# Optimization experiments

Measured on AMD Instinct MI355X. Metric: run time of the kernel, lower is better.

The kernel has to match this reference:

```python
import jax, jax.numpy as jnp
import numpy as np

G = 32               # sdf grid resolution (grid_size init default)
SCALE_FACTOR = 0.2   # forward default scale_factor
EPS = 1e-12


def setup_inputs() -> dict:
    key = jax.random.key(0)
    k1, k2 = jax.random.split(key)
    H, V, F = 2, 778, 1538  # two hands, MANO topology
    vertices = jax.random.normal(k1, (H, V, 3), dtype=jnp.float32)
    faces = jax.random.randint(k2, (F, 3), 0, V, dtype=jnp.int32)
    return {"vertices": vertices, "faces": faces}


def _sdiv(n, d):
    return n / jnp.where(jnp.abs(d) < EPS, EPS, d)


def _point_tri_dist2(p, a, b, c):
    # p: [P,1,3]; a,b,c: [1,F,3] -> squared distance [P,F] (Ericson closest-point)
    ab = b - a; ac = c - a; ap = p - a
    d1 = jnp.sum(ab * ap, -1); d2 = jnp.sum(ac * ap, -1)
    bp = p - b; d3 = jnp.sum(ab * bp, -1); d4 = jnp.sum(ac * bp, -1)
    cp = p - c; d5 = jnp.sum(ab * cp, -1); d6 = jnp.sum(ac * cp, -1)
    vc = d1 * d4 - d3 * d2
    vb = d5 * d2 - d1 * d6
    va = d3 * d6 - d5 * d4
    denom = va + vb + vc
    v_in = _sdiv(vb, denom); w_in = _sdiv(vc, denom)
    res = a + ab * v_in[..., None] + ac * w_in[..., None]  # face interior
    # edge BC
    cond = ((va <= 0) & ((d4 - d3) >= 0) & ((d5 - d6) >= 0))[..., None]
    w = _sdiv(d4 - d3, (d4 - d3) + (d5 - d6))[..., None]
    res = jnp.where(cond, b + (c - b) * w, res)
    # edge AC
    cond = ((vb <= 0) & (d2 >= 0) & (d6 <= 0))[..., None]
    w = _sdiv(d2, d2 - d6)[..., None]
    res = jnp.where(cond, a + ac * w, res)
    # edge AB
    cond = ((vc <= 0) & (d1 >= 0) & (d3 <= 0))[..., None]
    w = _sdiv(d1, d1 - d3)[..., None]
    res = jnp.where(cond, a + ab * w, res)
    # vertex regions (highest precedence)
    res = jnp.where(((d6 >= 0) & (d5 <= d6))[..., None], jnp.broadcast_to(c, res.shape), res)
    res = jnp.where(((d3 >= 0) & (d4 <= d3))[..., None], jnp.broadcast_to(b, res.shape), res)
    res = jnp.where(((d1 <= 0) & (d2 <= 0))[..., None], jnp.broadcast_to(a, res.shape), res)
    return jnp.sum((p - res) ** 2, -1)


def _inside(p, a, b, c):
    # parity of +x ray intersections (Moller-Trumbore with dir = (1,0,0))
    e1 = b - a; e2 = c - a
    det = e1[..., 1] * (-e2[..., 2]) + e1[..., 2] * e2[..., 1]  # dot(e1, cross(dir,e2))
    inv = _sdiv(1.0, det)
    s = p - a
    u = (s[..., 1] * (-e2[..., 2]) + s[..., 2] * e2[..., 1]) * inv
    q = jnp.cross(s, e1)
    v = q[..., 0] * inv                # dot(dir, q)
    t = jnp.sum(e2 * q, -1) * inv
    hit = (jnp.abs(det) > 1e-9) & (u >= 0) & (u <= 1) & (v >= 0) & (u + v <= 1) & (t > 0)
    return (jnp.sum(hit.astype(jnp.int32), axis=-1) % 2) == 1


def _sdf_grid(tri):
    # tri: [F,3,3] scaled triangles -> phi [G,G,G] laid out [z,y,x] (grid_sample DHW)
    a = tri[None, :, 0]; b = tri[None, :, 1]; c = tri[None, :, 2]
    lin = jnp.linspace(-1.0, 1.0, G, dtype=tri.dtype)
    zz, yy, xx = jnp.meshgrid(lin, lin, lin, indexing='ij')
    pts = jnp.stack([xx, yy, zz], -1).reshape(G, G * G, 3)  # chunk over z-slabs

    def slab(ps):
        p = ps[:, None, :]
        d2 = jnp.min(_point_tri_dist2(p, a, b, c), axis=1)
        ins = _inside(p, a, b, c)
        return jnp.where(ins, jnp.sqrt(jnp.maximum(d2, 0.0)), 0.0)

    return jax.lax.map(slab, pts).reshape(G, G, G)


def _trilinear(phi, coords):
    # grid_sample(align_corners=True, padding_mode='zeros'), coords [N,3] in xyz order
    g = G - 1
    f = (coords + 1.0) * 0.5 * g
    fx, fy, fz = f[:, 0], f[:, 1], f[:, 2]
    x0f = jnp.floor(fx); y0f = jnp.floor(fy); z0f = jnp.floor(fz)
    wx = fx - x0f; wy = fy - y0f; wz = fz - z0f
    x0 = x0f.astype(jnp.int32); y0 = y0f.astype(jnp.int32); z0 = z0f.astype(jnp.int32)

    def corner(zi, yi, xi, w):
        valid = (zi >= 0) & (zi <= g) & (yi >= 0) & (yi <= g) & (xi >= 0) & (xi <= g)
        val = phi[jnp.clip(zi, 0, g), jnp.clip(yi, 0, g), jnp.clip(xi, 0, g)]
        return jnp.where(valid, val, 0.0) * w

    out = (corner(z0, y0, x0, (1 - wz) * (1 - wy) * (1 - wx))
           + corner(z0, y0, x0 + 1, (1 - wz) * (1 - wy) * wx)
           + corner(z0, y0 + 1, x0, (1 - wz) * wy * (1 - wx))
           + corner(z0, y0 + 1, x0 + 1, (1 - wz) * wy * wx)
           + corner(z0 + 1, y0, x0, wz * (1 - wy) * (1 - wx))
           + corner(z0 + 1, y0, x0 + 1, wz * (1 - wy) * wx)
           + corner(z0 + 1, y0 + 1, x0, wz * wy * (1 - wx))
           + corner(z0 + 1, y0 + 1, x0 + 1, wz * wy * wx))
    return out


def reference(vertices, faces):
    H = vertices.shape[0]
    bmin = vertices.min(axis=1)   # [H,3]
    bmax = vertices.max(axis=1)
    center = jax.lax.stop_gradient(((bmin + bmax) * 0.5)[:, None, :])           # [H,1,3]
    scale = jax.lax.stop_gradient(
        ((1.0 + SCALE_FACTOR) * 0.5 * (bmax - bmin).max(-1))[:, None, None])    # [H,1,1]
    v_scaled = jax.lax.stop_gradient((vertices - center) / scale)
    tris = v_scaled[:, faces]                                                    # [H,F,3,3]
    phi = jax.lax.stop_gradient(jax.vmap(_sdf_grid)(tris))                       # [H,G,G,G]
    i = 1  # hardcoded loop 'for i in [1]' in the source
    coords = ((vertices - center[i][None]) / scale[i][None]).reshape(-1, 3)
    phi_val = _trilinear(phi[i], coords).reshape(H, -1)
    weights = jnp.ones((H, 1), dtype=vertices.dtype).at[i, 0].set(0.0)
    loss = jnp.sum(weights * phi_val) / (H ** 2)
    return loss
```

## Files before the change

### kernel.cpp

```cpp
#include <hip/hip_runtime.h>
#include <math.h>

#define NNODE 32768
#define NTHR  256
#define CHUNK 128
#define GY    160

__device__ __forceinline__ float rguard(float d) {
    float dd = (fabsf(d) < 1e-12f) ? 1e-12f : d;
    return __builtin_amdgcn_rcpf(dd);
}

__device__ __forceinline__ void cell_of(float px, float py, float pz,
                                        int& x0, int& y0, int& z0,
                                        float& wx, float& wy, float& wz) {
#pragma clang fp contract(off)
    float fx = (px + 1.0f) * 0.5f * 31.0f;
    float fy = (py + 1.0f) * 0.5f * 31.0f;
    float fz = (pz + 1.0f) * 0.5f * 31.0f;
    float x0f = floorf(fx), y0f = floorf(fy), z0f = floorf(fz);
    wx = fx - x0f; wy = fy - y0f; wz = fz - z0f;
    x0 = (int)fmaxf(fminf(x0f, 33.0f), -2.0f);
    y0 = (int)fmaxf(fminf(y0f, 33.0f), -2.0f);
    z0 = (int)fmaxf(fminf(z0f, 33.0f), -2.0f);
}

__device__ __forceinline__ void bbox_of(const float* __restrict__ verts, int V,
                                        float& ocx, float& ocy, float& ocz,
                                        float& osc) {
#pragma clang fp contract(off)
    const float* v1 = verts + (size_t)V * 3;
    float mn[3] = {1e30f, 1e30f, 1e30f};
    float mx[3] = {-1e30f, -1e30f, -1e30f};
    for (int i = threadIdx.x; i < V; i += blockDim.x) {
        for (int c = 0; c < 3; ++c) {
            float val = v1[i * 3 + c];
            mn[c] = fminf(mn[c], val);
            mx[c] = fmaxf(mx[c], val);
        }
    }
    for (int off = 32; off >= 1; off >>= 1) {
        for (int c = 0; c < 3; ++c) {
            mn[c] = fminf(mn[c], __shfl_down(mn[c], off));
            mx[c] = fmaxf(mx[c], __shfl_down(mx[c], off));
        }
    }
    __shared__ float smn[16][3], smx[16][3];
    int wv = threadIdx.x >> 6, lane = threadIdx.x & 63;
    if (lane == 0)
        for (int c = 0; c < 3; ++c) { smn[wv][c] = mn[c]; smx[wv][c] = mx[c]; }
    __syncthreads();
    const int nw = (int)blockDim.x >> 6;
    float ext = -1e30f, cc[3];
    for (int c = 0; c < 3; ++c) {
        float lo = 1e30f, hi = -1e30f;
        for (int w = 0; w < nw; ++w) {
            lo = fminf(lo, smn[w][c]);
            hi = fmaxf(hi, smx[w][c]);
        }
        cc[c] = (lo + hi) * 0.5f;
        ext = fmaxf(ext, hi - lo);
    }
    ocx = cc[0]; ocy = cc[1]; ocz = cc[2];
    osc = (1.0f + 0.2f) * 0.5f * ext;
    __syncthreads();
}

__device__ __forceinline__ void tri_node(
        float ax, float ay, float az, float abx, float aby, float abz,
        float acx, float acy, float acz, float inv, float det,
        float dbb, float dbc, float dcc,
        float px, float py, float pz, float& mind2, int& h) {
    float apx = px - ax, apy = py - ay, apz = pz - az;
    {
#pragma clang fp contract(fast)
        float d1 = abx * apx + aby * apy + abz * apz;
        float d2 = acx * apx + acy * apy + acz * apz;
        float d3 = d1 - dbb;
        float d4 = d2 - dbc;
        float d5 = d1 - dbc;
        float d6 = d2 - dcc;
        float vc = d1 * d4 - d3 * d2;
        float vb = d5 * d2 - d1 * d6;
        float va = d3 * d6 - d5 * d4;
        float denom = va + vb + vc;
        float rd = rguard(denom);
        float v_in = vb * rd, w_in = vc * rd;
        float rx = ax + abx * v_in + acx * w_in;
        float ry = ay + aby * v_in + acy * w_in;
        float rz = az + abz * v_in + acz * w_in;
        if (va <= 0.0f && (d4 - d3) >= 0.0f && (d5 - d6) >= 0.0f) {
            float w2 = (d4 - d3) * rguard((d4 - d3) + (d5 - d6));
            rx = ax + abx + (acx - abx) * w2;
            ry = ay + aby + (acy - aby) * w2;
            rz = az + abz + (acz - abz) * w2;
        }
        if (vb <= 0.0f && d2 >= 0.0f && d6 <= 0.0f) {
            float w2 = d2 * rguard(d2 - d6);
            rx = ax + acx * w2; ry = ay + acy * w2; rz = az + acz * w2;
        }
        if (vc <= 0.0f && d1 >= 0.0f && d3 <= 0.0f) {
            float w2 = d1 * rguard(d1 - d3);
            rx = ax + abx * w2; ry = ay + aby * w2; rz = az + abz * w2;
        }
        if (d6 >= 0.0f && d5 <= d6) { rx = ax + acx; ry = ay + acy; rz = az + acz; }
        if (d3 >= 0.0f && d4 <= d3) { rx = ax + abx; ry = ay + aby; rz = az + abz; }
        if (d1 <= 0.0f && d2 <= 0.0f) { rx = ax; ry = ay; rz = az; }
        float ddx = px - rx, ddy = py - ry, ddz = pz - rz;
        mind2 = fminf(mind2, ddx * ddx + ddy * ddy + ddz * ddz);
    }
    {
#pragma clang fp contract(off)
        float u = (apy * (-acz) + apz * acy) * inv;
        float qx = apy * abz - apz * aby;
        float qy = apz * abx - apx * abz;
        float qz = apx * aby - apy * abx;
        float v = qx * inv;
        float tt = (acx * qx + acy * qy + acz * qz) * inv;
        h += (fabsf(det) > 1e-9f && u >= 0.0f && u <= 1.0f && v >= 0.0f &&
              (u + v) <= 1.0f && tt > 0.0f) ? 1 : 0;
    }
}

__global__ void __launch_bounds__(NTHR) k_setup(
        const float* __restrict__ verts, const int* __restrict__ faces,
        float* __restrict__ tri, unsigned int* __restrict__ d2b,
        int* __restrict__ hits, int* __restrict__ cnt, int* __restrict__ list,
        int V, int F) {
    float cx0, cy0, cz0, sc;
    bbox_of(verts, V, cx0, cy0, cz0, sc);
    const int b = (int)blockIdx.x, tid = threadIdx.x;

    for (int t = b * NTHR + tid; t < NNODE; t += (int)gridDim.x * NTHR) {
        d2b[t] = 0xFFFFFFFFu;
        hits[t] = 0;
    }

    if (b == 0) {
        __shared__ unsigned bm[NNODE / 32];
        __shared__ int scnt[NTHR];
        for (int k = 0; k < 4; ++k) bm[tid * 4 + k] = 0u;
        __syncthreads();
        for (int i = tid; i < V; i += NTHR) {
#pragma clang fp contract(off)
            float px = (verts[i * 3 + 0] - cx0) / sc;
            float py = (verts[i * 3 + 1] - cy0) / sc;
            float pz = (verts[i * 3 + 2] - cz0) / sc;
            int x0, y0, z0; float wx, wy, wz;
            cell_of(px, py, pz, x0, y0, z0, wx, wy, wz);
            for (int k = 0; k < 8; ++k) {
                int zi = z0 + ((k >> 2) & 1), yi = y0 + ((k >> 1) & 1),
                    xi = x0 + (k & 1);
                if ((unsigned)zi < 32u && (unsigned)yi < 32u && (unsigned)xi < 32u) {
                    int node = (zi * 32 + yi) * 32 + xi;
                    atomicOr(&bm[node >> 5], 1u << (node & 31));
                }
            }
        }
        __syncthreads();
        unsigned w0 = bm[tid * 4 + 0], w1 = bm[tid * 4 + 1],
                 w2 = bm[tid * 4 + 2], w3 = bm[tid * 4 + 3];
        int c = __popc(w0) + __popc(w1) + __popc(w2) + __popc(w3);
        scnt[tid] = c;
        __syncthreads();
        for (int off = 1; off < NTHR; off <<= 1) {
            int v_ = (tid >= off) ? scnt[tid - off] : 0;
            __syncthreads();
            scnt[tid] += v_;
            __syncthreads();
        }
        if (tid == NTHR - 1) cnt[0] = scnt[NTHR - 1];
        int off = scnt[tid] - c;
        unsigned wsv[4] = {w0, w1, w2, w3};
        for (int k = 0; k < 4; ++k) {
            unsigned w = wsv[k];
            int basebit = (tid * 4 + k) * 32;
            while (w) {
                int bb = __ffs(w) - 1;
                list[off++] = basebit + bb;
                w &= w - 1;
            }
        }
    } else {
        int f = (b - 1) * NTHR + tid;
        if (f < F) {
#pragma clang fp contract(off)
            const float* v1 = verts + (size_t)V * 3;
            int i0 = faces[f * 3 + 0], i1 = faces[f * 3 + 1], i2 = faces[f * 3 + 2];
            float ax = (v1[i0 * 3 + 0] - cx0) / sc, ay = (v1[i0 * 3 + 1] - cy0) / sc,
                  az = (v1[i0 * 3 + 2] - cz0) / sc;
            float bx = (v1[i1 * 3 + 0] - cx0) / sc, by = (v1[i1 * 3 + 1] - cy0) / sc,
                  bz = (v1[i1 * 3 + 2] - cz0) / sc;
            float cx = (v1[i2 * 3 + 0] - cx0) / sc, cy = (v1[i2 * 3 + 1] - cy0) / sc,
                  cz = (v1[i2 * 3 + 2] - cz0) / sc;
            float abx = bx - ax, aby = by - ay, abz = bz - az;
            float acx = cx - ax, acy = cy - ay, acz = cz - az;
            float det = aby * (-acz) + abz * acy;
            float dd = (fabsf(det) < 1e-12f) ? 1e-12f : det;
            float inv = 1.0f / dd;
            float* r = tri + (size_t)f * 16;
            r[0] = ax;  r[1] = ay;  r[2] = az;
            r[3] = abx; r[4] = aby; r[5] = abz;
            r[6] = acx; r[7] = acy; r[8] = acz;
            r[9] = inv; r[10] = det;
            r[11] = abx * abx + aby * aby + abz * abz;
            r[12] = abx * acx + aby * acy + abz * acz;
            r[13] = acx * acx + acy * acy + acz * acz;
            r[14] = 0.0f; r[15] = 0.0f;
        }
    }
}

__global__ void __launch_bounds__(NTHR) k_main(
        const float* __restrict__ tri, const int* __restrict__ list,
        const int* __restrict__ cnt, unsigned int* __restrict__ d2b,
        int* __restrict__ hits, int F) {
    __shared__ float s[14][CHUNK];
    const int tid = threadIdx.x, lane = tid & 63, wv = tid >> 6;
    const int cbase = (int)blockIdx.x * CHUNK;
    const int tn = min(CHUNK, F - cbase);

    if (tid < tn) {
        const float4* g = (const float4*)(tri + (size_t)(cbase + tid) * 16);
        float4 r0 = g[0], r1 = g[1], r2 = g[2], r3 = g[3];
        s[0][tid] = r0.x;  s[1][tid] = r0.y;  s[2][tid] = r0.z;  s[3][tid] = r0.w;
        s[4][tid] = r1.x;  s[5][tid] = r1.y;  s[6][tid] = r1.z;  s[7][tid] = r1.w;
        s[8][tid] = r2.x;  s[9][tid] = r2.y;  s[10][tid] = r2.z; s[11][tid] = r2.w;
        s[12][tid] = r3.x; s[13][tid] = r3.y;
    }
    __syncthreads();

    const int n = cnt[0];
    const int ngroups = (n + 3) >> 2;
    for (int g = (int)blockIdx.y; g < ngroups; g += (int)gridDim.y) {
        const int idx = g * 4 + wv;
        if (idx >= n) continue;
        const int node = list[idx];
        float px, py, pz;
        {
#pragma clang fp contract(off)
            px = (float)((double)(node & 31) * (2.0 / 31.0) - 1.0);
            py = (float)((double)((node >> 5) & 31) * (2.0 / 31.0) - 1.0);
            pz = (float)((double)(node >> 10) * (2.0 / 31.0) - 1.0);
        }
        float m = 1e30f;
        int h = 0;
        for (int mi = 0; mi * 64 < tn; ++mi) {
            int j = lane + mi * 64;
            if (j < tn) {
                tri_node(s[0][j], s[1][j], s[2][j], s[3][j], s[4][j], s[5][j],
                         s[6][j], s[7][j], s[8][j], s[9][j], s[10][j],
                         s[11][j], s[12][j], s[13][j], px, py, pz, m, h);
            }
        }
        for (int off = 32; off >= 1; off >>= 1) {
            m = fminf(m, __shfl_xor(m, off));
            h += __shfl_xor(h, off);
        }
        if (lane == 0) {
            atomicMin(d2b + node, __float_as_uint(m));
            atomicAdd(hits + node, h);
        }
    }
}

__global__ void k_sum(const float* __restrict__ verts,
                      const unsigned int* __restrict__ d2b, const int* __restrict__ hits,
                      float* __restrict__ out, int V) {
    float cx, cy, cz, sc;
    bbox_of(verts, V, cx, cy, cz, sc);
    {
#pragma clang fp contract(off)
        __shared__ float sm[1024];
        const int tid = threadIdx.x;
        float val = 0.0f;
        for (int i = tid; i < V; i += 1024) {
            float px = (verts[i * 3 + 0] - cx) / sc;
            float py = (verts[i * 3 + 1] - cy) / sc;
            float pz = (verts[i * 3 + 2] - cz) / sc;
            int x0, y0, z0; float wx, wy, wz;
            cell_of(px, py, pz, x0, y0, z0, wx, wy, wz);
            auto corner = [&](int zi, int yi, int xi, float w) -> float {
#pragma clang fp contract(off)
                bool valid = (zi >= 0) && (zi <= 31) && (yi >= 0) && (yi <= 31) &&
                             (xi >= 0) && (xi <= 31);
                int zc = min(max(zi, 0), 31);
                int yc = min(max(yi, 0), 31);
                int xc = min(max(xi, 0), 31);
                int idx = (zc * 32 + yc) * 32 + xc;
                float vv = (hits[idx] & 1)
                               ? sqrtf(fmaxf(__uint_as_float(d2b[idx]), 0.0f))
                               : 0.0f;
                return valid ? vv * w : 0.0f;
            };
            val += corner(z0, y0, x0, (1.0f - wz) * (1.0f - wy) * (1.0f - wx))
                 + corner(z0, y0, x0 + 1, (1.0f - wz) * (1.0f - wy) * wx)
                 + corner(z0, y0 + 1, x0, (1.0f - wz) * wy * (1.0f - wx))
                 + corner(z0, y0 + 1, x0 + 1, (1.0f - wz) * wy * wx)
                 + corner(z0 + 1, y0, x0, wz * (1.0f - wy) * (1.0f - wx))
                 + corner(z0 + 1, y0, x0 + 1, wz * (1.0f - wy) * wx)
                 + corner(z0 + 1, y0 + 1, x0, wz * wy * (1.0f - wx))
                 + corner(z0 + 1, y0 + 1, x0 + 1, wz * wy * wx);
        }
        sm[tid] = val;
        __syncthreads();
        for (int ss = 512; ss >= 1; ss >>= 1) {
            if (tid < ss) sm[tid] += sm[tid + ss];
            __syncthreads();
        }
        if (tid == 0) out[0] = sm[0] * 0.25f;
    }
}

extern "C" void kernel_launch(void* const* d_in, const int* in_sizes, int n_in,
                              void* d_out, int out_size, void* d_ws, size_t ws_size,
                              hipStream_t stream) {
    const float* verts = (const float*)d_in[0];
    const int* faces = (const int*)d_in[1];
    float* out = (float*)d_out;
    float* ws = (float*)d_ws;

    int V = in_sizes[0] / 6;
    int F = in_sizes[1] / 3;

    float* tri = ws;
    unsigned int* d2b = (unsigned int*)(tri + 16 * (size_t)F);
    int* hits = (int*)(d2b + NNODE);
    int* cnt = hits + NNODE;
    int* list = cnt + 1;

    int nrec = (F + NTHR - 1) / NTHR;
    int nch = (F + CHUNK - 1) / CHUNK;

    k_setup<<<1 + nrec, NTHR, 0, stream>>>(verts, faces, tri, d2b, hits, cnt, list,
                                           V, F);
    k_main<<<dim3(nch, GY), NTHR, 0, stream>>>(tri, list, cnt, d2b, hits, F);
    k_sum<<<1, 1024, 0, stream>>>(verts, d2b, hits, out, V);
}
```

Baseline: 47.97 us.

## Keep one triangle per lane in registers and process two nodes per wave

The main kernel no longer stages 128-triangle chunks in shared memory. Each lane now holds one triangle in registers from a padded array of 64-face chunks, so the shared-memory reads and the block barrier go away. Each wave evaluates two grid nodes per iteration, and node coordinates are precomputed in setup into a float list instead of being rebuilt in double precision per node. Padding faces are placed far away so they never win the min or count as a hit. The cost is more atomics (twice as many blocks along x) and higher register pressure under the launch-bounds occupancy hint.

After: 67.40 us. 40.5% more time.

```diff
diff --git a/kernel.cpp b/kernel.cpp
--- a/kernel.cpp
+++ b/kernel.cpp
@@ -3,8 +3,7 @@
 
 #define NNODE 32768
 #define NTHR  256
-#define CHUNK 128
-#define GY    160
+#define GY2   82
 
 __device__ __forceinline__ float rguard(float d) {
     float dd = (fabsf(d) < 1e-12f) ? 1e-12f : d;
@@ -126,7 +125,7 @@
         const float* __restrict__ verts, const int* __restrict__ faces,
         float* __restrict__ tri, unsigned int* __restrict__ d2b,
         int* __restrict__ hits, int* __restrict__ cnt, int* __restrict__ list,
-        int V, int F) {
+        float* __restrict__ plist, int V, int F, int Fpad) {
     float cx0, cy0, cz0, sc;
     bbox_of(verts, V, cx0, cy0, cz0, sc);
     const int b = (int)blockIdx.x, tid = threadIdx.x;
@@ -177,7 +176,18 @@
             int basebit = (tid * 4 + k) * 32;
             while (w) {
                 int bb = __ffs(w) - 1;
-                list[off++] = basebit + bb;
+                int node = basebit + bb;
+                list[off] = node;
+                {
+#pragma clang fp contract(off)
+                    plist[off * 3 + 0] =
+                        (float)((double)(node & 31) * (2.0 / 31.0) - 1.0);
+                    plist[off * 3 + 1] =
+                        (float)((double)((node >> 5) & 31) * (2.0 / 31.0) - 1.0);
+                    plist[off * 3 + 2] =
+                        (float)((double)(node >> 10) * (2.0 / 31.0) - 1.0);
+                }
+                ++off;
                 w &= w - 1;
             }
         }
@@ -207,59 +217,56 @@
             r[12] = abx * acx + aby * acy + abz * acz;
             r[13] = acx * acx + acy * acy + acz * acz;
             r[14] = 0.0f; r[15] = 0.0f;
-        }
-    }
-}
-
-__global__ void __launch_bounds__(NTHR) k_main(
+        } else if (f < Fpad) {
+            float* r = tri + (size_t)f * 16;
+            r[0] = 100.0f; r[1] = 100.0f; r[2] = 100.0f;
+            for (int k = 3; k < 16; ++k) r[k] = 0.0f;
+        }
+    }
+}
+
+__global__ void __launch_bounds__(NTHR, 6) k_main(
         const float* __restrict__ tri, const int* __restrict__ list,
-        const int* __restrict__ cnt, unsigned int* __restrict__ d2b,
-        int* __restrict__ hits, int F) {
-    __shared__ float s[14][CHUNK];
-    const int tid = threadIdx.x, lane = tid & 63, wv = tid >> 6;
-    const int cbase = (int)blockIdx.x * CHUNK;
-    const int tn = min(CHUNK, F - cbase);
-
-    if (tid < tn) {
-        const float4* g = (const float4*)(tri + (size_t)(cbase + tid) * 16);
-        float4 r0 = g[0], r1 = g[1], r2 = g[2], r3 = g[3];
-        s[0][tid] = r0.x;  s[1][tid] = r0.y;  s[2][tid] = r0.z;  s[3][tid] = r0.w;
-        s[4][tid] = r1.x;  s[5][tid] = r1.y;  s[6][tid] = r1.z;  s[7][tid] = r1.w;
-        s[8][tid] = r2.x;  s[9][tid] = r2.y;  s[10][tid] = r2.z; s[11][tid] = r2.w;
-        s[12][tid] = r3.x; s[13][tid] = r3.y;
-    }
-    __syncthreads();
+        const float* __restrict__ plist, const int* __restrict__ cnt,
+        unsigned int* __restrict__ d2b, int* __restrict__ hits) {
+    const int lane = threadIdx.x & 63, wv = threadIdx.x >> 6;
+    const float4* g =
+        (const float4*)(tri + (size_t)((int)blockIdx.x * 64 + lane) * 16);
+    float4 r0 = g[0], r1 = g[1], r2 = g[2], r3 = g[3];
+    const float ax = r0.x, ay = r0.y, az = r0.z, abx = r0.w;
+    const float aby = r1.x, abz = r1.y, acx = r1.z, acy = r1.w;
+    const float acz = r2.x, inv = r2.y, det = r2.z, dbb = r2.w;
+    const float dbc = r3.x, dcc = r3.y;
 
     const int n = cnt[0];
-    const int ngroups = (n + 3) >> 2;
-    for (int g = (int)blockIdx.y; g < ngroups; g += (int)gridDim.y) {
-        const int idx = g * 4 + wv;
-        if (idx >= n) continue;
-        const int node = list[idx];
-        float px, py, pz;
-        {
-#pragma clang fp contract(off)
-            px = (float)((double)(node & 31) * (2.0 / 31.0) - 1.0);
-            py = (float)((double)((node >> 5) & 31) * (2.0 / 31.0) - 1.0);
-            pz = (float)((double)(node >> 10) * (2.0 / 31.0) - 1.0);
-        }
-        float m = 1e30f;
-        int h = 0;
-        for (int mi = 0; mi * 64 < tn; ++mi) {
-            int j = lane + mi * 64;
-            if (j < tn) {
-                tri_node(s[0][j], s[1][j], s[2][j], s[3][j], s[4][j], s[5][j],
-                         s[6][j], s[7][j], s[8][j], s[9][j], s[10][j],
-                         s[11][j], s[12][j], s[13][j], px, py, pz, m, h);
+    const int row = (int)blockIdx.y * 4 + wv;
+    const int nrow = (int)gridDim.y * 4;
+    for (int i = row * 2; i < n; i += nrow * 2) {
+        const bool two = (i + 1) < n;
+        float p0x = plist[i * 3 + 0], p0y = plist[i * 3 + 1],
+              p0z = plist[i * 3 + 2];
+        float p1x = 0, p1y = 0, p1z = 0;
+        if (two) {
+            p1x = plist[i * 3 + 3]; p1y = plist[i * 3 + 4]; p1z = plist[i * 3 + 5];
+        }
+        float m0 = 1e30f, m1 = 1e30f;
+        int h0 = 0, h1 = 0;
+        tri_node(ax, ay, az, abx, aby, abz, acx, acy, acz, inv, det,
+                 dbb, dbc, dcc, p0x, p0y, p0z, m0, h0);
+        if (two)
+            tri_node(ax, ay, az, abx, aby, abz, acx, acy, acz, inv, det,
+                     dbb, dbc, dcc, p1x, p1y, p1z, m1, h1);
+        for (int off = 32; off >= 1; off >>= 1) {
+            m0 = fminf(m0, __shfl_xor(m0, off)); h0 += __shfl_xor(h0, off);
+            m1 = fminf(m1, __shfl_xor(m1, off)); h1 += __shfl_xor(h1, off);
+        }
+        if (lane == 0) {
+            atomicMin(d2b + list[i], __float_as_uint(m0));
+            atomicAdd(hits + list[i], h0);
+            if (two) {
+                atomicMin(d2b + list[i + 1], __float_as_uint(m1));
+                atomicAdd(hits + list[i + 1], h1);
             }
-        }
-        for (int off = 32; off >= 1; off >>= 1) {
-            m = fminf(m, __shfl_xor(m, off));
-            h += __shfl_xor(h, off);
-        }
-        if (lane == 0) {
-            atomicMin(d2b + node, __float_as_uint(m));
-            atomicAdd(hits + node, h);
         }
     }
 }
@@ -322,18 +329,20 @@
 
     int V = in_sizes[0] / 6;
     int F = in_sizes[1] / 3;
+    int nch = (F + 63) / 64;
+    int Fpad = nch * 64;
 
     float* tri = ws;
-    unsigned int* d2b = (unsigned int*)(tri + 16 * (size_t)F);
+    unsigned int* d2b = (unsigned int*)(tri + 16 * (size_t)Fpad);
     int* hits = (int*)(d2b + NNODE);
     int* cnt = hits + NNODE;
     int* list = cnt + 1;
-
-    int nrec = (F + NTHR - 1) / NTHR;
-    int nch = (F + CHUNK - 1) / CHUNK;
+    float* plist = (float*)(list + NNODE);
+
+    int nrec = (Fpad + NTHR - 1) / NTHR;
 
     k_setup<<<1 + nrec, NTHR, 0, stream>>>(verts, faces, tri, d2b, hits, cnt, list,
-                                           V, F);
-    k_main<<<dim3(nch, GY), NTHR, 0, stream>>>(tri, list, cnt, d2b, hits, F);
+                                           plist, V, F, Fpad);
+    k_main<<<dim3(nch, GY2), NTHR, 0, stream>>>(tri, list, plist, cnt, d2b, hits);
     k_sum<<<1, 1024, 0, stream>>>(verts, d2b, hits, out, V);
 }
```
